# Kernel tuning notes

Hardware: AMD Instinct MI355X
Metric: run time of the kernel (lower is better)

The kernel has to match this reference:

```python
import jax, jax.numpy as jnp
import numpy as np

N_EMBD = 384
HEAD_SIZE = 64
BLOCK_SIZE = 64
SCALE = HEAD_SIZE * N_EMBD ** (-0.5)  # non-standard scale from source: k.shape[-1] * C**-0.5


def setup_inputs() -> dict:
    key = jax.random.key(0)
    kx, kk, kq, kv = jax.random.split(key, 4)
    B, T = 2048, BLOCK_SIZE
    x = jax.random.normal(kx, (B, T, N_EMBD), dtype=jnp.float32)
    # torch Linear(n_embd, head_size, bias=False): weight shape [head_size, n_embd], y = x @ W.T
    s = N_EMBD ** -0.5
    Wk = jax.random.uniform(kk, (HEAD_SIZE, N_EMBD), jnp.float32, -s, s)
    Wq = jax.random.uniform(kq, (HEAD_SIZE, N_EMBD), jnp.float32, -s, s)
    Wv = jax.random.uniform(kv, (HEAD_SIZE, N_EMBD), jnp.float32, -s, s)
    return {"x": x, "Wk": Wk, "Wq": Wq, "Wv": Wv}


def reference(x, Wk, Wq, Wv) -> jnp.ndarray:
    B, T, C = x.shape
    k = jnp.einsum("btc,hc->bth", x, Wk)  # [B,T,H]
    q = jnp.einsum("btc,hc->bth", x, Wq)
    v = jnp.einsum("btc,hc->bth", x, Wv)
    wei = jnp.einsum("bth,bsh->bts", q, k) * SCALE  # [B,T,T]
    causal = jnp.tril(jnp.ones((T, T), dtype=bool))
    wei = jnp.where(causal, wei, -jnp.inf)
    wei = jax.nn.softmax(wei, axis=-1)
    out = jnp.einsum("bts,bsh->bth", wei, v)  # [B,T,H]
    return out
```

## Files before the change

### kernel.cpp

```cpp
#include <hip/hip_runtime.h>

typedef _Float16 f16;
typedef _Float16 f16x8 __attribute__((ext_vector_type(8)));
typedef _Float16 f16x4 __attribute__((ext_vector_type(4)));
typedef float    f32x4 __attribute__((ext_vector_type(4)));

#define MFMA16(a, b, c) __builtin_amdgcn_mfma_f32_16x16x32_f16((a), (b), (c), 0, 0, 0)

constexpr int T = 64;
constexpr int C = 384;
constexpr int H = 64;
constexpr float SCALE = 3.26598632371090f;

__global__ void pack_w(const float* __restrict__ Wk, const float* __restrict__ Wq,
                       const float* __restrict__ Wv, f16* __restrict__ Wp) {
  int tid = blockIdx.x * blockDim.x + threadIdx.x;
  if (tid >= 3 * 12 * 4 * 64) return;
  int lane = tid & 63;
  int tile = tid >> 6;
  int ht = tile & 3;
  int kt = (tile >> 2) % 12;
  int wi = tile / 48;
  const float* W = (wi == 0) ? Wk : ((wi == 1) ? Wq : Wv);
  int h = 16 * ht + (lane & 15);
  int c = 32 * kt + 8 * (lane >> 4);
  const float* src = W + h * C + c;
  f16x8 v;
#pragma unroll
  for (int j = 0; j < 8; ++j) v[j] = (f16)src[j];
  *(f16x8*)(Wp + (size_t)tile * 512 + lane * 8) = v;
}

__global__ __launch_bounds__(256, 4) void head_fused(
    const float* __restrict__ x, const f16* __restrict__ Wp,
    float* __restrict__ out) {
  __shared__ f16 qp_lds[64][72];
  __shared__ f16 k_lds[64][72];
  __shared__ f16 vT_lds[64][72];

  const int b = blockIdx.x;
  const int tid = threadIdx.x;
  const int w = tid >> 6;
  const int lane = tid & 63;
  const int l15 = lane & 15;
  const int g = lane >> 4;
  const int t_ = 16 * w + l15;

  const f32x4 vzero = {0.0f, 0.0f, 0.0f, 0.0f};
  f32x4 accq[4], acck[4], accv[4];
#pragma unroll
  for (int i = 0; i < 4; ++i) { accq[i] = vzero; acck[i] = vzero; accv[i] = vzero; }

  const float* xrow = x + ((size_t)b * T + t_) * C;
  const f16* wp_lane = Wp + lane * 8;

  f32x4 pfa[2], pfb[2];
  pfa[0] = *(const f32x4*)(xrow + 0 * 32 + g * 8);
  pfb[0] = *(const f32x4*)(xrow + 0 * 32 + g * 8 + 4);
  pfa[1] = *(const f32x4*)(xrow + 1 * 32 + g * 8);
  pfb[1] = *(const f32x4*)(xrow + 1 * 32 + g * 8 + 4);

#pragma unroll
  for (int kt = 0; kt < 12; ++kt) {
    const f32x4 a0 = pfa[kt & 1];
    const f32x4 a1 = pfb[kt & 1];
    if (kt + 2 < 12) {
      pfa[kt & 1] = *(const f32x4*)(xrow + (kt + 2) * 32 + g * 8);
      pfb[kt & 1] = *(const f32x4*)(xrow + (kt + 2) * 32 + g * 8 + 4);
    }
    f16x8 xf;
#pragma unroll
    for (int j = 0; j < 4; ++j) { xf[j] = (f16)a0[j]; xf[4 + j] = (f16)a1[j]; }

    const f16* wk_base = wp_lane + (size_t)(0 * 12 + kt) * 4 * 512;
    const f16* wq_base = wp_lane + (size_t)(1 * 12 + kt) * 4 * 512;
    const f16* wv_base = wp_lane + (size_t)(2 * 12 + kt) * 4 * 512;
#pragma unroll
    for (int ht = 0; ht < 4; ++ht) {
      f16x8 wqf = *(const f16x8*)(wq_base + ht * 512);
      accq[ht] = MFMA16(wqf, xf, accq[ht]);
    }
#pragma unroll
    for (int ht = 0; ht < 4; ++ht) {
      f16x8 wkf = *(const f16x8*)(wk_base + ht * 512);
      acck[ht] = MFMA16(wkf, xf, acck[ht]);
    }
#pragma unroll
    for (int ht = 0; ht < 4; ++ht) {
      f16x8 wvf = *(const f16x8*)(wv_base + ht * 512);
      accv[ht] = MFMA16(xf, wvf, accv[ht]);
    }
  }

#pragma unroll
  for (int ht = 0; ht < 4; ++ht) {
    f16x4 pq, pk, pv;
#pragma unroll
    for (int r = 0; r < 4; ++r) {
      pq[r] = (f16)accq[ht][r];
      pk[r] = (f16)acck[ht][r];
      pv[r] = (f16)accv[ht][r];
    }
    *(f16x4*)&qp_lds[t_][16 * ht + 4 * g] = pq;
    *(f16x4*)&k_lds[t_][16 * ht + 4 * g] = pk;
    *(f16x4*)&vT_lds[16 * ht + l15][16 * w + 4 * g] = pv;
  }
  __syncthreads();

  f32x4 accs[4];
#pragma unroll
  for (int i = 0; i < 4; ++i) accs[i] = vzero;
#pragma unroll
  for (int kt = 0; kt < 2; ++kt) {
    f16x8 qf = *(const f16x8*)&qp_lds[t_][32 * kt + 8 * g];
#pragma unroll
    for (int mt = 0; mt < 4; ++mt) {
      f16x8 kf = *(const f16x8*)&k_lds[16 * mt + l15][32 * kt + 8 * g];
      accs[mt] = MFMA16(kf, qf, accs[mt]);
    }
  }

  float e[16];
  float mx = -__builtin_inff();
#pragma unroll
  for (int mt = 0; mt < 4; ++mt) {
#pragma unroll
    for (int r = 0; r < 4; ++r) {
      int s = 16 * mt + 4 * g + r;
      float lv = accs[mt][r] * SCALE;
      lv = (s <= t_) ? lv : -__builtin_inff();
      e[mt * 4 + r] = lv;
      mx = fmaxf(mx, lv);
    }
  }
  mx = fmaxf(mx, __shfl_xor(mx, 16));
  mx = fmaxf(mx, __shfl_xor(mx, 32));
  float sm = 0.0f;
#pragma unroll
  for (int i = 0; i < 16; ++i) { e[i] = __expf(e[i] - mx); sm += e[i]; }
  sm += __shfl_xor(sm, 16);
  sm += __shfl_xor(sm, 32);
  const float inv = 1.0f / sm;
#pragma unroll
  for (int mt = 0; mt < 4; ++mt) {
    f16x4 pp;
#pragma unroll
    for (int r = 0; r < 4; ++r) pp[r] = (f16)(e[mt * 4 + r] * inv);
    *(f16x4*)&qp_lds[t_][16 * mt + 4 * g] = pp;
  }

  f32x4 acco[4];
#pragma unroll
  for (int i = 0; i < 4; ++i) acco[i] = vzero;
#pragma unroll
  for (int kt = 0; kt < 2; ++kt) {
    f16x8 pf = *(const f16x8*)&qp_lds[t_][32 * kt + 8 * g];
#pragma unroll
    for (int mt = 0; mt < 4; ++mt) {
      f16x8 vf = *(const f16x8*)&vT_lds[16 * mt + l15][32 * kt + 8 * g];
      acco[mt] = MFMA16(vf, pf, acco[mt]);
    }
  }

  float* orow = out + ((size_t)b * T + t_) * H;
#pragma unroll
  for (int mt = 0; mt < 4; ++mt) {
    *(f32x4*)(orow + 16 * mt + 4 * g) = acco[mt];
  }
}

extern "C" void kernel_launch(void* const* d_in, const int* in_sizes, int n_in,
                              void* d_out, int out_size, void* d_ws, size_t ws_size,
                              hipStream_t stream) {
  const float* x  = (const float*)d_in[0];
  const float* Wk = (const float*)d_in[1];
  const float* Wq = (const float*)d_in[2];
  const float* Wv = (const float*)d_in[3];
  float* out = (float*)d_out;
  f16* Wp = (f16*)d_ws;

  pack_w<<<36, 256, 0, stream>>>(Wk, Wq, Wv, Wp);
  head_fused<<<2048, 256, 0, stream>>>(x, Wp, out);
}
```

Measured before the change: 333.7 us.

## Split QKV projection by output head tile per wave instead of by row

Each wave now computes three (matrix, head-tile) output combos across all 64 rows, instead of all 12 combos for its own 16 rows. Each weight fragment is loaded once per wave and reused across four row tiles, which cuts weight traffic fourfold. In exchange every wave now loads the full x tile, so x global/L2 reads go up fourfold per block, and the register-prefetch double buffering of x is dropped. Branches on wave-dependent matrix identity add some divergence-free but per-wave specialised code.

Measured after the change: 334.6 us. About the same (+0.3%).

```diff
diff --git a/kernel.cpp b/kernel.cpp
--- a/kernel.cpp
+++ b/kernel.cpp
@@ -47,63 +47,67 @@
   const int t_ = 16 * w + l15;
 
   const f32x4 vzero = {0.0f, 0.0f, 0.0f, 0.0f};
-  f32x4 accq[4], acck[4], accv[4];
+  f32x4 acc[3][4];
 #pragma unroll
-  for (int i = 0; i < 4; ++i) { accq[i] = vzero; acck[i] = vzero; accv[i] = vzero; }
+  for (int c = 0; c < 3; ++c)
+#pragma unroll
+    for (int tt = 0; tt < 4; ++tt) acc[c][tt] = vzero;
 
-  const float* xrow = x + ((size_t)b * T + t_) * C;
-  const f16* wp_lane = Wp + lane * 8;
+  const f16* wp_base[3];
+  bool isV[3];
+#pragma unroll
+  for (int c = 0; c < 3; ++c) {
+    int combo = 3 * w + c;
+    int m = combo >> 2;
+    int ht = combo & 3;
+    wp_base[c] = Wp + (size_t)(m * 48 + ht) * 512 + lane * 8;
+    isV[c] = (combo >= 8);
+  }
 
-  f32x4 pfa[2], pfb[2];
-  pfa[0] = *(const f32x4*)(xrow + 0 * 32 + g * 8);
-  pfb[0] = *(const f32x4*)(xrow + 0 * 32 + g * 8 + 4);
-  pfa[1] = *(const f32x4*)(xrow + 1 * 32 + g * 8);
-  pfb[1] = *(const f32x4*)(xrow + 1 * 32 + g * 8 + 4);
+  const float* xbase = x + (size_t)b * T * C;
 
 #pragma unroll
   for (int kt = 0; kt < 12; ++kt) {
-    const f32x4 a0 = pfa[kt & 1];
-    const f32x4 a1 = pfb[kt & 1];
-    if (kt + 2 < 12) {
-      pfa[kt & 1] = *(const f32x4*)(xrow + (kt + 2) * 32 + g * 8);
-      pfb[kt & 1] = *(const f32x4*)(xrow + (kt + 2) * 32 + g * 8 + 4);
-    }
-    f16x8 xf;
+    f16x8 xf[4];
 #pragma unroll
-    for (int j = 0; j < 4; ++j) { xf[j] = (f16)a0[j]; xf[4 + j] = (f16)a1[j]; }
-
-    const f16* wk_base = wp_lane + (size_t)(0 * 12 + kt) * 4 * 512;
-    const f16* wq_base = wp_lane + (size_t)(1 * 12 + kt) * 4 * 512;
-    const f16* wv_base = wp_lane + (size_t)(2 * 12 + kt) * 4 * 512;
+    for (int tt = 0; tt < 4; ++tt) {
+      const float* xr = xbase + (size_t)(16 * tt + l15) * C + kt * 32 + g * 8;
+      f32x4 a0 = *(const f32x4*)(xr);
+      f32x4 a1 = *(const f32x4*)(xr + 4);
 #pragma unroll
-    for (int ht = 0; ht < 4; ++ht) {
-      f16x8 wqf = *(const f16x8*)(wq_base + ht * 512);
-      accq[ht] = MFMA16(wqf, xf, accq[ht]);
+      for (int j = 0; j < 4; ++j) { xf[tt][j] = (f16)a0[j]; xf[tt][4 + j] = (f16)a1[j]; }
     }
 #pragma unroll
-    for (int ht = 0; ht < 4; ++ht) {
-      f16x8 wkf = *(const f16x8*)(wk_base + ht * 512);
-      acck[ht] = MFMA16(wkf, xf, acck[ht]);
-    }
+    for (int c = 0; c < 3; ++c) {
+      f16x8 wf = *(const f16x8*)(wp_base[c] + kt * 2048);
+      if (!isV[c]) {
 #pragma unroll
-    for (int ht = 0; ht < 4; ++ht) {
-      f16x8 wvf = *(const f16x8*)(wv_base + ht * 512);
-      accv[ht] = MFMA16(xf, wvf, accv[ht]);
+        for (int tt = 0; tt < 4; ++tt) acc[c][tt] = MFMA16(wf, xf[tt], acc[c][tt]);
+      } else {
+#pragma unroll
+        for (int tt = 0; tt < 4; ++tt) acc[c][tt] = MFMA16(xf[tt], wf, acc[c][tt]);
+      }
     }
   }
 
 #pragma unroll
-  for (int ht = 0; ht < 4; ++ht) {
-    f16x4 pq, pk, pv;
+  for (int c = 0; c < 3; ++c) {
+    int combo = 3 * w + c;
+    int m = combo >> 2;
+    int ht = combo & 3;
 #pragma unroll
-    for (int r = 0; r < 4; ++r) {
-      pq[r] = (f16)accq[ht][r];
-      pk[r] = (f16)acck[ht][r];
-      pv[r] = (f16)accv[ht][r];
+    for (int tt = 0; tt < 4; ++tt) {
+      f16x4 pd;
+#pragma unroll
+      for (int r = 0; r < 4; ++r) pd[r] = (f16)acc[c][tt][r];
+      if (m == 0) {
+        *(f16x4*)&k_lds[16 * tt + l15][16 * ht + 4 * g] = pd;
+      } else if (m == 1) {
+        *(f16x4*)&qp_lds[16 * tt + l15][16 * ht + 4 * g] = pd;
+      } else {
+        *(f16x4*)&vT_lds[16 * ht + l15][16 * tt + 4 * g] = pd;
+      }
     }
-    *(f16x4*)&qp_lds[t_][16 * ht + 4 * g] = pq;
-    *(f16x4*)&k_lds[t_][16 * ht + 4 * g] = pk;
-    *(f16x4*)&vT_lds[16 * ht + l15][16 * w + 4 * g] = pv;
   }
   __syncthreads();
 
```
